# Kernel tuning notes

Hardware: AMD Instinct MI355X
Metric: run time of the kernel (lower is better)

Reference implementation:

```python
import jax, jax.numpy as jnp
import numpy as np

# dims
B, S, D, H, NB = 2, 2048, 1024, 16, 32
DH = D // H          # 64 per-head dim
MLP = 4096
CLUSTER_SCORE = 0.1
LN_EPS = 1e-6


def _layernorm(x, g, b):
    mu = jnp.mean(x, axis=-1, keepdims=True)
    var = jnp.mean(jnp.square(x - mu), axis=-1, keepdims=True)
    return (x - mu) * jax.lax.rsqrt(var + LN_EPS) * g + b


def setup_inputs() -> dict:
    key = jax.random.key(0)
    ks = jax.random.split(key, 10)
    std = 0.02  # xl_init-style normal init scale
    return {
        "inputs": jax.random.normal(ks[0], (B, S, D), jnp.float32),
        "ln1_g": jnp.ones((D,), jnp.float32),
        "ln1_b": jnp.zeros((D,), jnp.float32),
        "Wq": jax.random.normal(ks[1], (D, H, DH), jnp.float32) * std,
        "Wk": jax.random.normal(ks[2], (D, H, DH), jnp.float32) * std,
        "Wv": jax.random.normal(ks[3], (D, H, DH), jnp.float32) * std,
        "Whq": jax.random.normal(ks[4], (H, DH, NB), jnp.float32) * std,
        "Whk": jax.random.normal(ks[5], (H, DH, NB), jnp.float32) * std,
        "Wo": jax.random.normal(ks[6], (H, DH, D), jnp.float32) * std,
        "ln2_g": jnp.ones((D,), jnp.float32),
        "ln2_b": jnp.zeros((D,), jnp.float32),
        "W1": jax.random.normal(ks[7], (D, MLP), jnp.float32) * std,
        "b1": jnp.zeros((MLP,), jnp.float32),
        "W2": jax.random.normal(ks[8], (MLP, D), jnp.float32) * std,
        "b2": jnp.zeros((D,), jnp.float32),
    }


def _lha_attention(x, Wq, Wk, Wv, Whq, Whk, Wo):
    # q,k,v: [B,S,H,DH]
    q = jnp.einsum("bsd,dhf->bshf", x, Wq)
    k = jnp.einsum("bsd,dhf->bshf", x, Wk)
    v = jnp.einsum("bsd,dhf->bshf", x, Wv)
    # learned-hash bucket assignment probabilities (lha_score_func='linear')
    qb = jax.nn.softmax(jnp.einsum("bshf,hfn->bshn", q, Whq), axis=-1)  # [B,S,H,NB]
    kb = jax.nn.softmax(jnp.einsum("bshf,hfn->bshn", k, Whk), axis=-1)
    # content scores + cluster (same-bucket) affinity term
    logits = jnp.einsum("bqhf,bkhf->bhqk", q, k) / jnp.sqrt(jnp.float32(DH))
    aff = jnp.einsum("bqhn,bkhn->bhqk", qb, kb)  # [B,H,S,S]
    logits = logits + CLUSTER_SCORE * aff
    attn = jax.nn.softmax(logits, axis=-1)
    out = jnp.einsum("bhqk,bkhf->bqhf", attn, v)
    out = jnp.einsum("bqhf,hfd->bqd", out, Wo)
    # auxiliary bucket load-balancing loss
    mq = jnp.mean(qb, axis=(0, 1))  # [H,NB]
    mk = jnp.mean(kb, axis=(0, 1))
    extra_loss = 0.5 * NB * (jnp.mean(jnp.sum(mq * mq, -1)) + jnp.mean(jnp.sum(mk * mk, -1)))
    return out, extra_loss


def reference(inputs, ln1_g, ln1_b, Wq, Wk, Wv, Whq, Whk, Wo,
              ln2_g, ln2_b, W1, b1, W2, b2):
    x = _layernorm(inputs, ln1_g, ln1_b)                      # pre-LN
    attn_out, extra_loss = _lha_attention(x, Wq, Wk, Wv, Whq, Whk, Wo)
    x = attn_out + inputs                                      # residual
    y = _layernorm(x, ln2_g, ln2_b)                            # pre-LN for MLP
    y = jax.nn.relu(jnp.einsum("bsd,dm->bsm", y, W1) + b1)
    y = jnp.einsum("bsm,md->bsd", y, W2) + b2
    return (x + y, extra_loss)
```

## Files before the change

### kernel.cpp

```cpp
#include <hip/hip_runtime.h>

typedef unsigned short u16;
typedef unsigned int u32;
typedef float f32x4 __attribute__((ext_vector_type(4)));
typedef short bf16x8 __attribute__((ext_vector_type(8)));

#define D_B 2
#define D_S 2048
#define D_D 1024
#define D_H 16
#define D_NB 32
#define D_DH 64
#define D_MLP 4096

__device__ __forceinline__ float bflo(u32 p) { union { u32 i; float f; } c; c.i = p << 16; return c.f; }
__device__ __forceinline__ float bfhi(u32 p) { union { u32 i; float f; } c; c.i = p & 0xffff0000u; return c.f; }
__device__ __forceinline__ u16 f2bf(float f) {
  union { float f; u32 i; } c; c.f = f;
  u32 x = c.i;
  u32 r = (x + 0x7fffu + ((x >> 16) & 1u)) >> 16;
  return (u16)r;
}
__device__ __forceinline__ u16 f2bf_fast(float f) {
  union { float f; u32 i; } c; c.f = f;
  return (u16)((c.i + 0x8000u) >> 16);
}
__device__ __forceinline__ u32 pack2(float lo, float hi) {
  return (u32)f2bf(lo) | ((u32)f2bf(hi) << 16);
}
__device__ __forceinline__ void unpack8(uint4 u, float* f) {
  f[0]=bflo(u.x); f[1]=bfhi(u.x); f[2]=bflo(u.y); f[3]=bfhi(u.y);
  f[4]=bflo(u.z); f[5]=bfhi(u.z); f[6]=bflo(u.w); f[7]=bfhi(u.w);
}
__device__ __forceinline__ bf16x8 scale_frag(uint4 u, float s) {
  float f[8]; unpack8(u, f);
  uint4 r;
  r.x = pack2(f[0]*s, f[1]*s); r.y = pack2(f[2]*s, f[3]*s);
  r.z = pack2(f[4]*s, f[5]*s); r.w = pack2(f[6]*s, f[7]*s);
  union { uint4 u; bf16x8 v; } c; c.u = r; return c.v;
}
__device__ __forceinline__ bf16x8 as_frag(uint4 u) {
  union { uint4 u; bf16x8 v; } c; c.u = u; return c.v;
}
__device__ __forceinline__ void gl_lds16(const u16* g, u16* l) {
  __builtin_amdgcn_global_load_lds((const __attribute__((address_space(1))) void*)g,
                                   (__attribute__((address_space(3))) void*)l, 16, 0, 0);
}

__device__ __forceinline__ void tr64(const float* __restrict__ W, u16* __restrict__ WT,
                                     int K, int N, int k0, int n0, int t) {
  __shared__ float tile[64][65];
  int tx = t & 15, ty = t >> 4;
  #pragma unroll
  for (int i = 0; i < 4; i++) {
    float4 v = *reinterpret_cast<const float4*>(W + (size_t)(k0 + ty * 4 + i) * N + n0 + tx * 4);
    tile[ty * 4 + i][tx * 4 + 0] = v.x;
    tile[ty * 4 + i][tx * 4 + 1] = v.y;
    tile[ty * 4 + i][tx * 4 + 2] = v.z;
    tile[ty * 4 + i][tx * 4 + 3] = v.w;
  }
  __syncthreads();
  #pragma unroll
  for (int i = 0; i < 4; i++) {
    int n = ty * 4 + i;
    uint2 o;
    o.x = pack2(tile[tx*4+0][n], tile[tx*4+1][n]);
    o.y = pack2(tile[tx*4+2][n], tile[tx*4+3][n]);
    *reinterpret_cast<uint2*>(WT + (size_t)(n0 + n) * K + k0 + tx * 4) = o;
  }
}

__global__ __launch_bounds__(256) void prep1_kernel(const float* __restrict__ Wq,
                                                    const float* __restrict__ Wk,
                                                    const float* __restrict__ Wv,
                                                    const float* __restrict__ Wo,
                                                    u16* __restrict__ wqkvT,
                                                    u16* __restrict__ woT,
                                                    float* __restrict__ mqmk) {
  int bid = blockIdx.x, t = threadIdx.x;
  if (bid >= 1024) {
    reinterpret_cast<float4*>(mqmk)[t] = make_float4(0.f, 0.f, 0.f, 0.f);
    return;
  }
  const float* W; u16* WT;
  int sub = bid & 255;
  int k0 = (sub >> 4) * 64, n0 = (sub & 15) * 64;
  if (bid < 256)      { W = Wq; WT = wqkvT; }
  else if (bid < 512) { W = Wk; WT = wqkvT + 1024 * 1024; }
  else if (bid < 768) { W = Wv; WT = wqkvT + 2048 * 1024; }
  else                { W = Wo; WT = woT; }
  tr64(W, WT, 1024, 1024, k0, n0, t);
}

__global__ __launch_bounds__(256) void prep2_kernel(const float* __restrict__ W1,
                                                    const float* __restrict__ W2,
                                                    u16* __restrict__ w1T,
                                                    u16* __restrict__ w2T) {
  int bid = blockIdx.x, t = threadIdx.x;
  if (bid < 1024) {
    int n0 = (bid & 63) * 64, k0 = (bid >> 6) * 64;
    tr64(W1, w1T, 1024, 4096, k0, n0, t);
  } else {
    int i = bid - 1024;
    int n0 = (i & 15) * 64, k0 = (i >> 4) * 64;
    tr64(W2, w2T, 4096, 1024, k0, n0, t);
  }
}

__global__ __launch_bounds__(256) void ln_kernel(const float* __restrict__ x,
                                                 const float* __restrict__ g,
                                                 const float* __restrict__ bta,
                                                 u16* __restrict__ out) {
  int row = blockIdx.x, t = threadIdx.x;
  float4 v = reinterpret_cast<const float4*>(x + (size_t)row * D_D)[t];
  float s = v.x + v.y + v.z + v.w;
  float q = v.x*v.x + v.y*v.y + v.z*v.z + v.w*v.w;
  #pragma unroll
  for (int o = 32; o; o >>= 1) { s += __shfl_down(s, o); q += __shfl_down(q, o); }
  __shared__ float rs[4], rq[4];
  if ((t & 63) == 0) { rs[t >> 6] = s; rq[t >> 6] = q; }
  __syncthreads();
  s = rs[0] + rs[1] + rs[2] + rs[3];
  q = rq[0] + rq[1] + rq[2] + rq[3];
  float mu   = s * (1.0f / 1024.0f);
  float var  = fmaxf(q * (1.0f / 1024.0f) - mu * mu, 0.0f);
  float rstd = rsqrtf(var + 1e-6f);
  float4 gg = reinterpret_cast<const float4*>(g)[t];
  float4 bb = reinterpret_cast<const float4*>(bta)[t];
  float o0 = (v.x - mu) * rstd * gg.x + bb.x;
  float o1 = (v.y - mu) * rstd * gg.y + bb.y;
  float o2 = (v.z - mu) * rstd * gg.z + bb.z;
  float o3 = (v.w - mu) * rstd * gg.w + bb.w;
  uint2 w; w.x = pack2(o0, o1); w.y = pack2(o2, o3);
  reinterpret_cast<uint2*>(out + (size_t)row * D_D)[t] = w;
}

__global__ __launch_bounds__(256, 2) void gemm_bt(const u16* __restrict__ A,
                                                  const u16* __restrict__ Bt,
                                                  u16* __restrict__ Cq,
                                                  u16* __restrict__ Ck,
                                                  u16* __restrict__ Cv,
                                                  int M, int N, int K, int ldb) {
  __shared__ u16 As[128 * 32];
  __shared__ u16 Bs[128 * 32];
  const int t = threadIdx.x, w = t >> 6, lane = t & 63;
  const int quad = lane >> 4, l16 = lane & 15;
  const int m0 = blockIdx.y * 128, n0 = blockIdx.x * 128;
  const int wm = (w >> 1) * 64, wn = (w & 1) * 64;

  f32x4 acc[4][4];
  #pragma unroll
  for (int i = 0; i < 4; i++)
    #pragma unroll
    for (int n = 0; n < 4; n++) acc[i][n] = (f32x4){0.f, 0.f, 0.f, 0.f};

  const int srow = lane >> 2, scol = (lane & 3) * 8;
  const u16* ag0 = A  + (size_t)(m0 + w * 32 + srow) * K + scol;
  const u16* ag1 = ag0 + (size_t)16 * K;
  const u16* bg0 = Bt + (size_t)(n0 + w * 32 + srow) * ldb + scol;
  const u16* bg1 = bg0 + (size_t)16 * ldb;
  u16* al0 = As + w * 1024;
  u16* bl0 = Bs + w * 1024;

  for (int k0 = 0; k0 < K; k0 += 32) {
    gl_lds16(ag0 + k0, al0);
    gl_lds16(ag1 + k0, al0 + 512);
    gl_lds16(bg0 + k0, bl0);
    gl_lds16(bg1 + k0, bl0 + 512);
    __syncthreads();
    bf16x8 af[4], bf[4];
    #pragma unroll
    for (int i = 0; i < 4; i++)
      af[i] = *reinterpret_cast<const bf16x8*>(As + (wm + i * 16 + l16) * 32 + quad * 8);
    #pragma unroll
    for (int n = 0; n < 4; n++)
      bf[n] = *reinterpret_cast<const bf16x8*>(Bs + (wn + n * 16 + l16) * 32 + quad * 8);
    #pragma unroll
    for (int i = 0; i < 4; i++)
      #pragma unroll
      for (int n = 0; n < 4; n++)
        acc[i][n] = __builtin_amdgcn_mfma_f32_16x16x32_bf16(af[i], bf[n], acc[i][n], 0, 0, 0);
    __syncthreads();
  }

  #pragma unroll
  for (int i = 0; i < 4; i++) {
    #pragma unroll
    for (int r = 0; r < 4; r++) {
      const int m = m0 + wm + i * 16 + quad * 4 + r;
      #pragma unroll
      for (int nt = 0; nt < 4; nt++) {
        const int n = n0 + wn + nt * 16 + l16;
        float v = acc[i][nt][r];
        const int sel = n >> 10, nn = n & 1023;
        const int h = nn >> 6, f = nn & 63;
        const int b = m >> 11, s = m & 2047;
        const size_t bh = (size_t)(b * D_H + h);
        if (sel == 0)      Cq[(bh * D_S + s) * 96 + f] = f2bf(v);
        else if (sel == 1) Ck[(bh * D_S + s) * 96 + f] = f2bf(v);
        else               Cv[(bh * 64 + f) * D_S + s] = f2bf(v);
      }
    }
  }
}

__global__ __launch_bounds__(256, 2) void gemm_bt64(const u16* __restrict__ A,
                                                    const u16* __restrict__ Bt,
                                                    const float* __restrict__ bias,
                                                    const float* __restrict__ resid,
                                                    void* __restrict__ C,
                                                    int M, int N, int K, int ldb,
                                                    int do_relu, int out_f32) {
  __shared__ u16 As[64 * 32];
  __shared__ u16 Bs[128 * 32];
  const int t = threadIdx.x, w = t >> 6, lane = t & 63;
  const int quad = lane >> 4, l16 = lane & 15;
  const int m0 = blockIdx.y * 64, n0 = blockIdx.x * 128;
  const int wm = (w >> 1) * 32, wn = (w & 1) * 64;

  f32x4 acc[2][4];
  #pragma unroll
  for (int i = 0; i < 2; i++)
    #pragma unroll
    for (int n = 0; n < 4; n++) acc[i][n] = (f32x4){0.f, 0.f, 0.f, 0.f};

  const int srow = lane >> 2, scol = (lane & 3) * 8;
  const u16* ag0 = A  + (size_t)(m0 + w * 16 + srow) * K + scol;
  const u16* bg0 = Bt + (size_t)(n0 + w * 32 + srow) * ldb + scol;
  const u16* bg1 = bg0 + (size_t)16 * ldb;
  u16* al0 = As + w * 512;
  u16* bl0 = Bs + w * 1024;

  for (int k0 = 0; k0 < K; k0 += 32) {
    gl_lds16(ag0 + k0, al0);
    gl_lds16(bg0 + k0, bl0);
    gl_lds16(bg1 + k0, bl0 + 512);
    __syncthreads();
    bf16x8 af[2], bf[4];
    #pragma unroll
    for (int i = 0; i < 2; i++)
      af[i] = *reinterpret_cast<const bf16x8*>(As + (wm + i * 16 + l16) * 32 + quad * 8);
    #pragma unroll
    for (int n = 0; n < 4; n++)
      bf[n] = *reinterpret_cast<const bf16x8*>(Bs + (wn + n * 16 + l16) * 32 + quad * 8);
    #pragma unroll
    for (int i = 0; i < 2; i++)
      #pragma unroll
      for (int n = 0; n < 4; n++)
        acc[i][n] = __builtin_amdgcn_mfma_f32_16x16x32_bf16(af[i], bf[n], acc[i][n], 0, 0, 0);
    __syncthreads();
  }

  #pragma unroll
  for (int i = 0; i < 2; i++) {
    #pragma unroll
    for (int r = 0; r < 4; r++) {
      const int m = m0 + wm + i * 16 + quad * 4 + r;
      #pragma unroll
      for (int nt = 0; nt < 4; nt++) {
        const int n = n0 + wn + nt * 16 + l16;
        float v = acc[i][nt][r];
        if (bias)    v += bias[n];
        if (do_relu) v  = fmaxf(v, 0.0f);
        if (resid)   v += resid[(size_t)m * N + n];
        if (out_f32) reinterpret_cast<float*>(C)[(size_t)m * N + n] = v;
        else         reinterpret_cast<u16*>(C)[(size_t)m * N + n]   = f2bf(v);
      }
    }
  }
}

__global__ __launch_bounds__(256) void bucket2_kernel(u16* __restrict__ qp,
                                                      const float* __restrict__ Whq,
                                                      float* __restrict__ mq,
                                                      u16* __restrict__ kp,
                                                      const float* __restrict__ Whk,
                                                      float* __restrict__ mk) {
  const int bx = blockIdx.x;
  const int side = bx >> 8;
  u16* P        = side ? kp  : qp;
  const float* Wh = side ? Whk : Whq;
  float* acc    = side ? mk  : mq;
  const float sscale = side ? 1.0f : 0.1f;
  const int id = bx & 255;
  const int bh = id >> 3, chunk = id & 7;
  const int h = bh & 15;
  const int t = threadIdx.x, w = t >> 6, lane = t & 63;
  const int rsub = lane >> 5;
  const int b = lane & 31;

  __shared__ float WhL[32 * 65];
  __shared__ float qs[4][2][64];
  __shared__ float accL[32];

  #pragma unroll
  for (int i = 0; i < 8; i++) {
    int idx = t * 8 + i;
    WhL[(idx & 31) * 65 + (idx >> 5)] = Wh[h * 2048 + idx];
  }
  if (t < 32) accL[t] = 0.f;
  __syncthreads();

  float whr[64];
  #pragma unroll
  for (int i = 0; i < 16; i++) {
    float4 v = *reinterpret_cast<const float4*>(&WhL[b * 65 + i * 4]);
    whr[i*4+0] = v.x; whr[i*4+1] = v.y; whr[i*4+2] = v.z; whr[i*4+3] = v.w;
  }

  float racc = 0.f;
  const int row0 = bh * 2048 + chunk * 256;
  for (int it = 0; it < 32; it++) {
    const int rr = row0 + it * 8 + w * 2 + rsub;
    u16* qrow = P + (size_t)rr * 96;
    u32 u = *reinterpret_cast<const u32*>(qrow + b * 2);
    *reinterpret_cast<float2*>(&qs[w][rsub][b * 2]) = make_float2(bflo(u), bfhi(u));
    float s0 = 0.f, s1 = 0.f, s2 = 0.f, s3 = 0.f;
    #pragma unroll
    for (int i = 0; i < 16; i++) {
      float4 qv = *reinterpret_cast<const float4*>(&qs[w][rsub][i * 4]);
      s0 = fmaf(qv.x, whr[i*4+0], s0);
      s1 = fmaf(qv.y, whr[i*4+1], s1);
      s2 = fmaf(qv.z, whr[i*4+2], s2);
      s3 = fmaf(qv.w, whr[i*4+3], s3);
    }
    float l = (s0 + s1) + (s2 + s3);
    float m = l;
    m = fmaxf(m, __shfl_xor(m, 1));  m = fmaxf(m, __shfl_xor(m, 2));
    m = fmaxf(m, __shfl_xor(m, 4));  m = fmaxf(m, __shfl_xor(m, 8));
    m = fmaxf(m, __shfl_xor(m, 16));
    float e = __expf(fminf(l - m, 0.0f));
    float ss = e;
    ss += __shfl_xor(ss, 1);  ss += __shfl_xor(ss, 2);
    ss += __shfl_xor(ss, 4);  ss += __shfl_xor(ss, 8);
    ss += __shfl_xor(ss, 16);
    float p = e / fmaxf(ss, 1e-20f);
    qrow[64 + b] = f2bf(p * sscale);
    racc += p;
  }
  atomicAdd(&accL[b], racc);
  __syncthreads();
  if (t < 32) atomicAdd(&acc[h * D_NB + t], accL[t]);
}

__global__ __launch_bounds__(256, 2) void attn_kernel(const u16* __restrict__ qp,
                                                      const u16* __restrict__ kp,
                                                      const u16* __restrict__ vt,
                                                      u16* __restrict__ out) {
  const int bh = blockIdx.y;
  const int s0 = blockIdx.x * 64;
  const int h = bh & 15, b = bh >> 4;
  const int t = threadIdx.x, w = t >> 6, lane = t & 63;
  const int quad = lane >> 4, l16 = lane & 15;
  const int qh = w & 1, kvh = w >> 1;

  __shared__ u16 Ks[2][64 * 104];
  __shared__ u16 Vs[2][64 * 72];
  __shared__ u16 Ps[4][32 * 88];
  __shared__ float Lb[64];

  bf16x8 Qf[2][3];
  #pragma unroll
  for (int m = 0; m < 2; m++) {
    const u16* qr = qp + ((size_t)bh * D_S + s0 + qh * 32 + m * 16 + l16) * 96;
    #pragma unroll
    for (int kg = 0; kg < 3; kg++) {
      uint4 u = *reinterpret_cast<const uint4*>(qr + kg * 32 + quad * 8);
      Qf[m][kg] = (kg < 2) ? scale_frag(u, 0.125f) : as_frag(u);
    }
  }

  f32x4 Oa[2][4];
  float lp[2][4];
  #pragma unroll
  for (int m = 0; m < 2; m++)
    #pragma unroll
    for (int f = 0; f < 4; f++) Oa[m][f] = (f32x4){0.f,0.f,0.f,0.f};
  #pragma unroll
  for (int m = 0; m < 2; m++)
    #pragma unroll
    for (int r = 0; r < 4; r++) lp[m][r] = 0.f;

  const int srow = t >> 2, seg = t & 3;
  const u16* kgp = kp + ((size_t)bh * D_S + srow) * 96 + seg * 24;
  const u16* vgp = vt + ((size_t)bh * 64 + srow) * D_S + seg * 16;
  u16* kd0 = &Ks[0][srow * 104 + seg * 24];
  u16* kd1 = &Ks[1][srow * 104 + seg * 24];
  u16* vd0 = &Vs[0][srow * 72 + seg * 16];
  u16* vd1 = &Vs[1][srow * 72 + seg * 16];

  for (int kt = 0; kt < 16; kt++) {
    __syncthreads();
    {
      const u16* ka = kgp + (size_t)(kt * 64) * 96;
      const u16* kb = kgp + (size_t)(1024 + kt * 64) * 96;
      #pragma unroll
      for (int j = 0; j < 3; j++) {
        *reinterpret_cast<uint4*>(kd0 + j * 8) = *reinterpret_cast<const uint4*>(ka + j * 8);
        *reinterpret_cast<uint4*>(kd1 + j * 8) = *reinterpret_cast<const uint4*>(kb + j * 8);
      }
      const u16* va = vgp + kt * 64;
      const u16* vb = vgp + 1024 + kt * 64;
      #pragma unroll
      for (int j = 0; j < 2; j++) {
        *reinterpret_cast<uint4*>(vd0 + j * 8) = *reinterpret_cast<const uint4*>(va + j * 8);
        *reinterpret_cast<uint4*>(vd1 + j * 8) = *reinterpret_cast<const uint4*>(vb + j * 8);
      }
    }
    __syncthreads();

    f32x4 S[2][4];
    #pragma unroll
    for (int m = 0; m < 2; m++)
      #pragma unroll
      for (int n = 0; n < 4; n++) S[m][n] = (f32x4){0.f,0.f,0.f,0.f};
    #pragma unroll
    for (int n = 0; n < 4; n++) {
      bf16x8 Bk[3];
      #pragma unroll
      for (int kg = 0; kg < 3; kg++)
        Bk[kg] = *reinterpret_cast<const bf16x8*>(&Ks[kvh][(n * 16 + l16) * 104 + kg * 32 + quad * 8]);
      #pragma unroll
      for (int m = 0; m < 2; m++)
        #pragma unroll
        for (int kg = 0; kg < 3; kg++)
          S[m][n] = __builtin_amdgcn_mfma_f32_16x16x32_bf16(Qf[m][kg], Bk[kg], S[m][n], 0, 0, 0);
    }

    #pragma unroll
    for (int m = 0; m < 2; m++) {
      #pragma unroll
      for (int r = 0; r < 4; r++) {
        const int row = m * 16 + quad * 4 + r;
        u16* pw = &Ps[w][row * 88 + ((row >> 3) & 1) * 16 + l16];
        float es = 0.f;
        #pragma unroll
        for (int n = 0; n < 4; n++) {
          float e = __expf(fminf(S[m][n][r], 30.0f));
          es += e;
          pw[n * 16] = f2bf_fast(e);
        }
        lp[m][r] += es;
      }
    }
    asm volatile("s_waitcnt lgkmcnt(0)" ::: "memory");

    #pragma unroll
    for (int m = 0; m < 2; m++) {
      const int row = m * 16 + l16;
      bf16x8 Pa[2];
      #pragma unroll
      for (int kg = 0; kg < 2; kg++)
        Pa[kg] = *reinterpret_cast<const bf16x8*>(&Ps[w][row * 88 + ((row >> 3) & 1) * 16 + kg * 32 + quad * 8]);
      #pragma unroll
      for (int f = 0; f < 4; f++)
        #pragma unroll
        for (int kg = 0; kg < 2; kg++) {
          bf16x8 Bv = *reinterpret_cast<const bf16x8*>(&Vs[kvh][(f * 16 + l16) * 72 + kg * 32 + quad * 8]);
          Oa[m][f] = __builtin_amdgcn_mfma_f32_16x16x32_bf16(Pa[kg], Bv, Oa[m][f], 0, 0, 0);
        }
    }
  }

  float lpr[2][4];
  #pragma unroll
  for (int m = 0; m < 2; m++)
    #pragma unroll
    for (int r = 0; r < 4; r++) {
      float v = lp[m][r];
      v += __shfl_xor(v, 1); v += __shfl_xor(v, 2);
      v += __shfl_xor(v, 4); v += __shfl_xor(v, 8);
      lpr[m][r] = v;
    }

  __syncthreads();
  float* Ob = reinterpret_cast<float*>(&Ks[0][0]);
  if (kvh == 1) {
    #pragma unroll
    for (int m = 0; m < 2; m++)
      #pragma unroll
      for (int r = 0; r < 4; r++) {
        const int row = qh * 32 + m * 16 + quad * 4 + r;
        if (l16 == 0) Lb[row] = lpr[m][r];
        #pragma unroll
        for (int f = 0; f < 4; f++)
          Ob[row * 68 + f * 16 + l16] = Oa[m][f][r];
      }
  }
  __syncthreads();
  if (kvh == 0) {
    #pragma unroll
    for (int m = 0; m < 2; m++)
      #pragma unroll
      for (int r = 0; r < 4; r++) {
        const int row = qh * 32 + m * 16 + quad * 4 + r;
        float ltot = lpr[m][r] + Lb[row];
        float inv = 1.0f / fmaxf(ltot, 1e-20f);
        #pragma unroll
        for (int f = 0; f < 4; f++) {
          float val = (Oa[m][f][r] + Ob[row * 68 + f * 16 + l16]) * inv;
          out[((size_t)(b * D_S + s0 + row) * D_H + h) * 64 + f * 16 + l16] = f2bf(val);
        }
      }
  }
}

__global__ __launch_bounds__(256) void loss_kernel(const float* __restrict__ mq,
                                                   const float* __restrict__ mk,
                                                   float* __restrict__ out) {
  int t = threadIdx.x;
  float s = 0.0f;
  for (int i = t; i < 512; i += 256) {
    float a = mq[i] * (1.0f / 4096.0f);
    float c = mk[i] * (1.0f / 4096.0f);
    s += a * a + c * c;
  }
  #pragma unroll
  for (int o = 32; o; o >>= 1) s += __shfl_xor(s, o);
  __shared__ float r[4];
  if ((t & 63) == 0) r[t >> 6] = s;
  __syncthreads();
  if (t == 0) out[0] = r[0] + r[1] + r[2] + r[3];
}

extern "C" void kernel_launch(void* const* d_in, const int* in_sizes, int n_in,
                              void* d_out, int out_size, void* d_ws, size_t ws_size,
                              hipStream_t stream) {
  const float* inp  = (const float*)d_in[0];
  const float* ln1g = (const float*)d_in[1];
  const float* ln1b = (const float*)d_in[2];
  const float* Wq   = (const float*)d_in[3];
  const float* Wk   = (const float*)d_in[4];
  const float* Wv   = (const float*)d_in[5];
  const float* Whq  = (const float*)d_in[6];
  const float* Whk  = (const float*)d_in[7];
  const float* Wo   = (const float*)d_in[8];
  const float* ln2g = (const float*)d_in[9];
  const float* ln2b = (const float*)d_in[10];
  const float* W1   = (const float*)d_in[11];
  const float* b1   = (const float*)d_in[12];
  const float* W2   = (const float*)d_in[13];
  const float* b2   = (const float*)d_in[14];
  float* out = (float*)d_out;

  char* w = (char*)d_ws;
  u16* wqkvT = (u16*)(w + 0);
  u16* woT   = (u16*)(w + 6291456);
  u16* qp    = (u16*)(w + 8388608);
  u16* kp    = (u16*)(w + 20971520);
  u16* xhat  = (u16*)(w + 33554432);
  u16* attnb = xhat;
  float* mq  = (float*)(w + 41943040);
  float* mk  = mq + 512;
  u16* yhat  = (u16*)(w + 0);
  u16* w1T   = (u16*)(w + 8388608);
  u16* w2T   = (u16*)(w + 16777216);
  u16* h1    = (u16*)(w + 25165824);
  u16* vt    = (u16*)d_out;

  prep1_kernel<<<dim3(1025), dim3(256), 0, stream>>>(Wq, Wk, Wv, Wo, wqkvT, woT, mq);
  ln_kernel<<<dim3(4096), dim3(256), 0, stream>>>(inp, ln1g, ln1b, xhat);
  gemm_bt<<<dim3(24, 32), dim3(256), 0, stream>>>(xhat, wqkvT, qp, kp, vt, 4096, 3072, 1024, 1024);
  bucket2_kernel<<<dim3(512), dim3(256), 0, stream>>>(qp, Whq, mq, kp, Whk, mk);
  attn_kernel<<<dim3(32, 32), dim3(256), 0, stream>>>(qp, kp, vt, attnb);
  prep2_kernel<<<dim3(2048), dim3(256), 0, stream>>>(W1, W2, w1T, w2T);
  gemm_bt64<<<dim3(8, 64), dim3(256), 0, stream>>>(attnb, woT, nullptr, inp,
                                                   out, 4096, 1024, 1024, 1024, 0, 1);
  ln_kernel<<<dim3(4096), dim3(256), 0, stream>>>(out, ln2g, ln2b, yhat);
  gemm_bt64<<<dim3(16, 64), dim3(256), 0, stream>>>(yhat, w1T, b1, nullptr,
                                                    h1, 4096, 2048, 1024, 1024, 1, 0);
  gemm_bt64<<<dim3(8, 64), dim3(256), 0, stream>>>(h1, w2T, b2, out,
                                                   out, 4096, 1024, 2048, 4096, 0, 1);
  gemm_bt64<<<dim3(16, 64), dim3(256), 0, stream>>>(yhat, w1T + (size_t)2048 * 1024, b1 + 2048, nullptr,
                                                    h1, 4096, 2048, 1024, 1024, 1, 0);
  gemm_bt64<<<dim3(8, 64), dim3(256), 0, stream>>>(h1, w2T + 2048, nullptr, out,
                                                   out, 4096, 1024, 2048, 4096, 0, 1);
  loss_kernel<<<dim3(1), dim3(256), 0, stream>>>(mq, mk, out + 4194304);
}
```

Baseline: 484.8 us.

## Restructure attention loop: register-prefetch K, direct V fragments, transposed S, exp2

```diff
diff --git a/kernel.cpp b/kernel.cpp
--- a/kernel.cpp
+++ b/kernel.cpp
@@ -1,4 +1,5 @@
 #include <hip/hip_runtime.h>
+#include <hip/hip_bf16.h>
 
 typedef unsigned short u16;
 typedef unsigned int u32;
@@ -12,6 +13,7 @@
 #define D_NB 32
 #define D_DH 64
 #define D_MLP 4096
+#define LOG2E 1.4426950408889634f
 
 __device__ __forceinline__ float bflo(u32 p) { union { u32 i; float f; } c; c.i = p << 16; return c.f; }
 __device__ __forceinline__ float bfhi(u32 p) { union { u32 i; float f; } c; c.i = p & 0xffff0000u; return c.f; }
@@ -21,12 +23,12 @@
   u32 r = (x + 0x7fffu + ((x >> 16) & 1u)) >> 16;
   return (u16)r;
 }
-__device__ __forceinline__ u16 f2bf_fast(float f) {
-  union { float f; u32 i; } c; c.f = f;
-  return (u16)((c.i + 0x8000u) >> 16);
-}
 __device__ __forceinline__ u32 pack2(float lo, float hi) {
   return (u32)f2bf(lo) | ((u32)f2bf(hi) << 16);
+}
+__device__ __forceinline__ u32 pk_bf16(float lo, float hi) {
+  __hip_bfloat162 h = __float22bfloat162_rn(make_float2(lo, hi));
+  union { __hip_bfloat162 h; u32 u; } c; c.h = h; return c.u;
 }
 __device__ __forceinline__ void unpack8(uint4 u, float* f) {
   f[0]=bflo(u.x); f[1]=bfhi(u.x); f[2]=bflo(u.y); f[3]=bfhi(u.y);
@@ -135,7 +137,7 @@
   reinterpret_cast<uint2*>(out + (size_t)row * D_D)[t] = w;
 }
 
-__global__ __launch_bounds__(256, 2) void gemm_bt(const u16* __restrict__ A,
+__global__ __launch_bounds__(256, 3) void gemm_bt(const u16* __restrict__ A,
                                                   const u16* __restrict__ Bt,
                                                   u16* __restrict__ Cq,
                                                   u16* __restrict__ Ck,
@@ -204,7 +206,7 @@
   }
 }
 
-__global__ __launch_bounds__(256, 2) void gemm_bt64(const u16* __restrict__ A,
+__global__ __launch_bounds__(256, 4) void gemm_bt64(const u16* __restrict__ A,
                                                     const u16* __restrict__ Bt,
                                                     const float* __restrict__ bias,
                                                     const float* __restrict__ resid,
@@ -281,7 +283,7 @@
   u16* P        = side ? kp  : qp;
   const float* Wh = side ? Whk : Whq;
   float* acc    = side ? mk  : mq;
-  const float sscale = side ? 1.0f : 0.1f;
+  const float sscale = side ? 1.0f : 0.1f * LOG2E;
   const int id = bx & 255;
   const int bh = id >> 3, chunk = id & 7;
   const int h = bh & 15;
@@ -343,7 +345,7 @@
   if (t < 32) atomicAdd(&acc[h * D_NB + t], accL[t]);
 }
 
-__global__ __launch_bounds__(256, 2) void attn_kernel(const u16* __restrict__ qp,
+__global__ __launch_bounds__(256, 3) void attn_kernel(const u16* __restrict__ qp,
                                                       const u16* __restrict__ kp,
                                                       const u16* __restrict__ vt,
                                                       u16* __restrict__ out) {
@@ -355,9 +357,8 @@
   const int qh = w & 1, kvh = w >> 1;
 
   __shared__ u16 Ks[2][64 * 104];
-  __shared__ u16 Vs[2][64 * 72];
-  __shared__ u16 Ps[4][32 * 88];
-  __shared__ float Lb[64];
+  __shared__ u16 Ps[4][32 * 72];
+  __shared__ float Laux[2][64];
 
   bf16x8 Qf[2][3];
   #pragma unroll
@@ -366,140 +367,132 @@
     #pragma unroll
     for (int kg = 0; kg < 3; kg++) {
       uint4 u = *reinterpret_cast<const uint4*>(qr + kg * 32 + quad * 8);
-      Qf[m][kg] = (kg < 2) ? scale_frag(u, 0.125f) : as_frag(u);
+      Qf[m][kg] = (kg < 2) ? scale_frag(u, 0.125f * LOG2E) : as_frag(u);
     }
   }
 
   f32x4 Oa[2][4];
-  float lp[2][4];
+  float lp[2];
   #pragma unroll
   for (int m = 0; m < 2; m++)
     #pragma unroll
     for (int f = 0; f < 4; f++) Oa[m][f] = (f32x4){0.f,0.f,0.f,0.f};
-  #pragma unroll
-  for (int m = 0; m < 2; m++)
-    #pragma unroll
-    for (int r = 0; r < 4; r++) lp[m][r] = 0.f;
+  lp[0] = 0.f; lp[1] = 0.f;
 
   const int srow = t >> 2, seg = t & 3;
   const u16* kgp = kp + ((size_t)bh * D_S + srow) * 96 + seg * 24;
-  const u16* vgp = vt + ((size_t)bh * 64 + srow) * D_S + seg * 16;
   u16* kd0 = &Ks[0][srow * 104 + seg * 24];
   u16* kd1 = &Ks[1][srow * 104 + seg * 24];
-  u16* vd0 = &Vs[0][srow * 72 + seg * 16];
-  u16* vd1 = &Vs[1][srow * 72 + seg * 16];
+  const u16* vbase = vt + ((size_t)bh * 64 + l16) * D_S + kvh * 1024 + quad * 8;
+
+  uint4 kr0[3], kr1[3];
+  {
+    const u16* ka = kgp;
+    const u16* kb = kgp + (size_t)1024 * 96;
+    #pragma unroll
+    for (int j = 0; j < 3; j++) {
+      kr0[j] = *reinterpret_cast<const uint4*>(ka + j * 8);
+      kr1[j] = *reinterpret_cast<const uint4*>(kb + j * 8);
+    }
+  }
 
   for (int kt = 0; kt < 16; kt++) {
     __syncthreads();
-    {
-      const u16* ka = kgp + (size_t)(kt * 64) * 96;
-      const u16* kb = kgp + (size_t)(1024 + kt * 64) * 96;
+    #pragma unroll
+    for (int j = 0; j < 3; j++) {
+      *reinterpret_cast<uint4*>(kd0 + j * 8) = kr0[j];
+      *reinterpret_cast<uint4*>(kd1 + j * 8) = kr1[j];
+    }
+    if (kt < 15) {
+      const u16* ka = kgp + (size_t)((kt + 1) * 64) * 96;
+      const u16* kb = kgp + (size_t)(1024 + (kt + 1) * 64) * 96;
       #pragma unroll
       for (int j = 0; j < 3; j++) {
-        *reinterpret_cast<uint4*>(kd0 + j * 8) = *reinterpret_cast<const uint4*>(ka + j * 8);
-        *reinterpret_cast<uint4*>(kd1 + j * 8) = *reinterpret_cast<const uint4*>(kb + j * 8);
+        kr0[j] = *reinterpret_cast<const uint4*>(ka + j * 8);
+        kr1[j] = *reinterpret_cast<const uint4*>(kb + j * 8);
       }
-      const u16* va = vgp + kt * 64;
-      const u16* vb = vgp + 1024 + kt * 64;
-      #pragma unroll
-      for (int j = 0; j < 2; j++) {
-        *reinterpret_cast<uint4*>(vd0 + j * 8) = *reinterpret_cast<const uint4*>(va + j * 8);
-        *reinterpret_cast<uint4*>(vd1 + j * 8) = *reinterpret_cast<const uint4*>(vb + j * 8);
-      }
     }
     __syncthreads();
 
-    f32x4 S[2][4];
-    #pragma unroll
-    for (int m = 0; m < 2; m++)
-      #pragma unroll
-      for (int n = 0; n < 4; n++) S[m][n] = (f32x4){0.f,0.f,0.f,0.f};
-    #pragma unroll
-    for (int n = 0; n < 4; n++) {
-      bf16x8 Bk[3];
+    bf16x8 Bv[4][2];
+    #pragma unroll
+    for (int ft = 0; ft < 4; ft++)
+      #pragma unroll
+      for (int kb2 = 0; kb2 < 2; kb2++)
+        Bv[ft][kb2] = *reinterpret_cast<const bf16x8*>(vbase + (size_t)ft * 16 * D_S + kt * 64 + kb2 * 32);
+
+    #pragma unroll
+    for (int mt = 0; mt < 4; mt++) {
+      bf16x8 Kf[3];
       #pragma unroll
       for (int kg = 0; kg < 3; kg++)
-        Bk[kg] = *reinterpret_cast<const bf16x8*>(&Ks[kvh][(n * 16 + l16) * 104 + kg * 32 + quad * 8]);
-      #pragma unroll
-      for (int m = 0; m < 2; m++)
+        Kf[kg] = *reinterpret_cast<const bf16x8*>(&Ks[kvh][(mt * 16 + l16) * 104 + kg * 32 + quad * 8]);
+      #pragma unroll
+      for (int nt = 0; nt < 2; nt++) {
+        f32x4 ST = (f32x4){0.f,0.f,0.f,0.f};
         #pragma unroll
         for (int kg = 0; kg < 3; kg++)
-          S[m][n] = __builtin_amdgcn_mfma_f32_16x16x32_bf16(Qf[m][kg], Bk[kg], S[m][n], 0, 0, 0);
-    }
-
-    #pragma unroll
-    for (int m = 0; m < 2; m++) {
-      #pragma unroll
-      for (int r = 0; r < 4; r++) {
-        const int row = m * 16 + quad * 4 + r;
-        u16* pw = &Ps[w][row * 88 + ((row >> 3) & 1) * 16 + l16];
-        float es = 0.f;
+          ST = __builtin_amdgcn_mfma_f32_16x16x32_bf16(Kf[kg], Qf[nt][kg], ST, 0, 0, 0);
+        float e0 = exp2f(ST[0]), e1 = exp2f(ST[1]), e2 = exp2f(ST[2]), e3 = exp2f(ST[3]);
+        lp[nt] += (e0 + e1) + (e2 + e3);
+        uint2 pk; pk.x = pk_bf16(e0, e1); pk.y = pk_bf16(e2, e3);
+        *reinterpret_cast<uint2*>(&Ps[w][(nt * 16 + l16) * 72 + mt * 16 + quad * 4]) = pk;
+      }
+    }
+    asm volatile("s_waitcnt lgkmcnt(0)" ::: "memory");
+
+    #pragma unroll
+    for (int nt = 0; nt < 2; nt++) {
+      bf16x8 Pa[2];
+      #pragma unroll
+      for (int kb2 = 0; kb2 < 2; kb2++)
+        Pa[kb2] = *reinterpret_cast<const bf16x8*>(&Ps[w][(nt * 16 + l16) * 72 + kb2 * 32 + quad * 8]);
+      #pragma unroll
+      for (int ft = 0; ft < 4; ft++)
         #pragma unroll
-        for (int n = 0; n < 4; n++) {
-          float e = __expf(fminf(S[m][n][r], 30.0f));
-          es += e;
-          pw[n * 16] = f2bf_fast(e);
-        }
-        lp[m][r] += es;
-      }
-    }
-    asm volatile("s_waitcnt lgkmcnt(0)" ::: "memory");
-
-    #pragma unroll
-    for (int m = 0; m < 2; m++) {
-      const int row = m * 16 + l16;
-      bf16x8 Pa[2];
-      #pragma unroll
-      for (int kg = 0; kg < 2; kg++)
-        Pa[kg] = *reinterpret_cast<const bf16x8*>(&Ps[w][row * 88 + ((row >> 3) & 1) * 16 + kg * 32 + quad * 8]);
-      #pragma unroll
-      for (int f = 0; f < 4; f++)
-        #pragma unroll
-        for (int kg = 0; kg < 2; kg++) {
-          bf16x8 Bv = *reinterpret_cast<const bf16x8*>(&Vs[kvh][(f * 16 + l16) * 72 + kg * 32 + quad * 8]);
-          Oa[m][f] = __builtin_amdgcn_mfma_f32_16x16x32_bf16(Pa[kg], Bv, Oa[m][f], 0, 0, 0);
-        }
-    }
-  }
-
-  float lpr[2][4];
-  #pragma unroll
-  for (int m = 0; m < 2; m++)
-    #pragma unroll
-    for (int r = 0; r < 4; r++) {
-      float v = lp[m][r];
-      v += __shfl_xor(v, 1); v += __shfl_xor(v, 2);
-      v += __shfl_xor(v, 4); v += __shfl_xor(v, 8);
-      lpr[m][r] = v;
-    }
-
-  __syncthreads();
+        for (int kb2 = 0; kb2 < 2; kb2++)
+          Oa[nt][ft] = __builtin_amdgcn_mfma_f32_16x16x32_bf16(Pa[kb2], Bv[ft][kb2], Oa[nt][ft], 0, 0, 0);
+    }
+  }
+
+  float lpr[2];
+  #pragma unroll
+  for (int nt = 0; nt < 2; nt++) {
+    float v = lp[nt];
+    v += __shfl_xor(v, 16); v += __shfl_xor(v, 32);
+    lpr[nt] = v;
+  }
+
+  __syncthreads();
+  if (quad == 0) {
+    Laux[kvh][qh * 32 + 0 * 16 + l16] = lpr[0];
+    Laux[kvh][qh * 32 + 1 * 16 + l16] = lpr[1];
+  }
   float* Ob = reinterpret_cast<float*>(&Ks[0][0]);
   if (kvh == 1) {
     #pragma unroll
-    for (int m = 0; m < 2; m++)
+    for (int nt = 0; nt < 2; nt++)
       #pragma unroll
       for (int r = 0; r < 4; r++) {
-        const int row = qh * 32 + m * 16 + quad * 4 + r;
-        if (l16 == 0) Lb[row] = lpr[m][r];
+        const int row = qh * 32 + nt * 16 + quad * 4 + r;
         #pragma unroll
-        for (int f = 0; f < 4; f++)
-          Ob[row * 68 + f * 16 + l16] = Oa[m][f][r];
+        for (int ft = 0; ft < 4; ft++)
+          Ob[row * 68 + ft * 16 + l16] = Oa[nt][ft][r];
       }
   }
   __syncthreads();
   if (kvh == 0) {
     #pragma unroll
-    for (int m = 0; m < 2; m++)
+    for (int nt = 0; nt < 2; nt++)
       #pragma unroll
       for (int r = 0; r < 4; r++) {
-        const int row = qh * 32 + m * 16 + quad * 4 + r;
-        float ltot = lpr[m][r] + Lb[row];
+        const int row = qh * 32 + nt * 16 + quad * 4 + r;
+        float ltot = Laux[0][row] + Laux[1][row];
         float inv = 1.0f / fmaxf(ltot, 1e-20f);
         #pragma unroll
-        for (int f = 0; f < 4; f++) {
-          float val = (Oa[m][f][r] + Ob[row * 68 + f * 16 + l16]) * inv;
-          out[((size_t)(b * D_S + s0 + row) * D_H + h) * 64 + f * 16 + l16] = f2bf(val);
+        for (int ft = 0; ft < 4; ft++) {
+          float val = (Oa[nt][ft][r] + Ob[row * 68 + ft * 16 + l16]) * inv;
+          out[((size_t)(b * D_S + s0 + row) * D_H + h) * 64 + ft * 16 + l16] = f2bf(val);
         }
       }
   }
```

New measurement: 570.3 us. 1.18x slower.
